# Optimization experiments

Measured on AMD Instinct MI355X. Metric: run time of the kernel, lower is better.

## Reference

```python
import jax, jax.numpy as jnp
import numpy as np

B, S, N = 64, 256, 512


def setup_inputs() -> dict:
    key = jax.random.key(0)
    ks = jax.random.split(key, 8)
    x = jax.random.normal(ks[0], (B, S, N), dtype=jnp.float32)
    # sparse adjacency, no self loops (module assumes adj has no self-loop)
    adj = (jax.random.uniform(ks[1], (N, N)) < 0.05).astype(jnp.float32)
    adj = adj * (1.0 - jnp.eye(N, dtype=jnp.float32))
    W = jax.random.uniform(ks[2], (N, N), dtype=jnp.float32)  # torch.rand init
    parent_node_weigh = jax.random.uniform(ks[3], (N,), dtype=jnp.float32)
    bound = 1.0 / np.sqrt(N)  # torch Linear default init
    Wq_w = jax.random.uniform(ks[4], (N, N), minval=-bound, maxval=bound, dtype=jnp.float32)
    Wq_b = jax.random.uniform(ks[5], (N,), minval=-bound, maxval=bound, dtype=jnp.float32)
    Wk_w = jax.random.uniform(ks[6], (N, N), minval=-bound, maxval=bound, dtype=jnp.float32)
    Wk_b = jax.random.uniform(ks[7], (N,), minval=-bound, maxval=bound, dtype=jnp.float32)
    return {"x": x, "adj": adj, "W": W, "parent_node_weigh": parent_node_weigh,
            "Wq_w": Wq_w, "Wq_b": Wq_b, "Wk_w": Wk_w, "Wk_b": Wk_b}


def reference(x, adj, W, parent_node_weigh, Wq_w, Wq_b, Wk_w, Wk_b):
    # x: (B,S,N). Q,K = Linear(x).permute(0,2,1) -> (B,N,S)
    Q = jnp.einsum('bsk,nk->bns', x, Wq_w) + Wq_b[None, :, None]
    K = jnp.einsum('bsk,nk->bns', x, Wk_w) + Wk_b[None, :, None]
    xt = jnp.transpose(x, (0, 2, 1))  # (B,N,S)
    n = adj.shape[0]
    # Algebraic equivalent of the repeat/mask/matmul/bmm chain:
    # Att[b,m,n] = adj[m,n] * sum_j W[m,j] * adj[j,n] * <K[b,j,:], Q[b,n,:]>
    S_kq = jnp.einsum('bjs,bns->bjn', K, Q)  # (B,N,N)
    Att = adj * jnp.einsum('mj,bjn->bmn', W, adj[:, :, None].transpose(2, 0, 1)[0][None] * S_kq if False else adj[None, :, :] * S_kq)
    Att = Att + jnp.diag(parent_node_weigh)[None, :, :]
    cycle_adj = jnp.eye(n, dtype=adj.dtype) + adj
    Att = jax.nn.softmax(Att, axis=1) * cycle_adj  # softmax over dim=1 (torch dim=1)
    agg_x = jnp.einsum('bmn,bms->bns', Att, xt)  # Att^T @ x
    return (agg_x, Att)
```

## Files before the change

kernel.cpp:

```cpp
#include <hip/hip_runtime.h>
#include <hip/hip_fp16.h>
#include <cstdint>
#include <cmath>

#define BB 64
#define SS 256
#define NN 512
#define MAXC 64

typedef float f32x4 __attribute__((ext_vector_type(4)));
typedef _Float16 half8 __attribute__((ext_vector_type(8)));
typedef _Float16 h2 __attribute__((ext_vector_type(2)));

__device__ __forceinline__ unsigned short f2h(float f) {
  return __half_as_ushort(__float2half(f));
}
__device__ __forceinline__ h2 u2h2(uint32_t u) {
  union { uint32_t u; h2 h; } c; c.u = u; return c.h;
}
__device__ __forceinline__ float2 unpackh2(uint32_t u) {
  return make_float2(__half2float(__ushort_as_half((unsigned short)(u & 0xffffu))),
                     __half2float(__ushort_as_half((unsigned short)(u >> 16))));
}

__device__ __forceinline__ void gload_lds16(const void* g, void* s) {
  __builtin_amdgcn_global_load_lds(
      (const __attribute__((address_space(1))) uint32_t*)g,
      (__attribute__((address_space(3))) uint32_t*)s, 16, 0, 0);
}

__global__ __launch_bounds__(256) void k_collist(const float* __restrict__ adj,
                                                 int* __restrict__ col_idx,
                                                 int* __restrict__ col_cnt) {
  const int n = blockIdx.x * 4 + (threadIdx.x >> 6);
  const int lane = threadIdx.x & 63;
  int cnt = 0;
  for (int m0 = 0; m0 < NN; m0 += 64) {
    const int m = m0 + lane;
    const float a = adj[(size_t)m * NN + n];
    unsigned long long mask = __ballot(a != 0.0f);
    const int prefix = __popcll(mask & ((1ull << lane) - 1ull));
    if (a != 0.0f && cnt + prefix < MAXC) col_idx[n * MAXC + cnt + prefix] = m;
    cnt += __popcll(mask);
  }
  if (lane == 0) col_cnt[n] = (cnt > MAXC) ? MAXC : cnt;
}

__global__ __launch_bounds__(256) void k_wsub(const float* __restrict__ W,
                                              const int* __restrict__ col_idx,
                                              const int* __restrict__ col_cnt,
                                              int* __restrict__ col_off,
                                              float* __restrict__ Wsub) {
  const int n = blockIdx.x;
  const int t = threadIdx.x;
  const int wave = t >> 6, lane = t & 63;
  __shared__ int lsh[MAXC];
  __shared__ int preSh;
  const int c = col_cnt[n];
  if (wave == 0) {
    int pre = 0;
#pragma unroll
    for (int i0 = 0; i0 < NN; i0 += 64) {
      const int i = i0 + lane;
      const int cc = col_cnt[i];
      pre += (i < n) ? cc * cc : 0;
    }
#pragma unroll
    for (int off = 32; off; off >>= 1) pre += __shfl_xor(pre, off);
    if (lane == 0) { col_off[n] = pre; preSh = pre; }
    if (lane < c) lsh[lane] = col_idx[n * MAXC + lane];
  }
  __syncthreads();
  if (lane < c) {
    const float* Wm = W + (size_t)lsh[lane] * NN;
    float* dst = Wsub + preSh + lane;
    for (int ji = wave; ji < c; ji += 4)
      dst[(size_t)ji * c] = Wm[lsh[ji]];
  }
}

__global__ __launch_bounds__(256) void k_xprep(const float* __restrict__ x,
                                               unsigned short* __restrict__ xp,
                                               unsigned short* __restrict__ xt,
                                               float* __restrict__ Att) {
  __shared__ float tile[32][33];
  const int b = blockIdx.z;
  const int s0 = blockIdx.x * 32, n0 = blockIdx.y * 32;
  const float* xb = x + (size_t)b * SS * NN;
  const int tx = threadIdx.x, ty = threadIdx.y;
#pragma unroll
  for (int i = ty; i < 32; i += 8) {
    const float v = xb[(size_t)(s0 + i) * NN + n0 + tx];
    tile[i][tx] = v;
    xp[(size_t)(b * SS + s0 + i) * 512 + n0 + tx] = f2h(v);
  }
  {
    const int bid = (blockIdx.z * 16 + blockIdx.y) * 8 + blockIdx.x;
    const int t = ty * 32 + tx;
    f32x4* dst = (f32x4*)(Att + (size_t)bid * 2048);
    const f32x4 z = (f32x4)0.0f;
    dst[t] = z;
    dst[t + 256] = z;
  }
  __syncthreads();
  unsigned short* xtb = xt + (size_t)b * NN * SS;
#pragma unroll
  for (int i = ty; i < 32; i += 8)
    xtb[(size_t)(n0 + i) * SS + s0 + tx] = f2h(tile[tx][i]);
}

__global__ __launch_bounds__(128) void k_wsplit(const float* __restrict__ Wq,
                                                const float* __restrict__ Wk,
                                                unsigned short* __restrict__ Wqp,
                                                unsigned short* __restrict__ Wkp) {
  const int n = blockIdx.x;
  const float* src = blockIdx.y ? Wk : Wq;
  unsigned short* dst = blockIdx.y ? Wkp : Wqp;
  const int k = threadIdx.x * 4;
  float4 v = *(const float4*)(src + (size_t)n * NN + k);
  ushort4 o;
  o.x = f2h(v.x); o.y = f2h(v.y); o.z = f2h(v.z); o.w = f2h(v.w);
  *(ushort4*)(dst + (size_t)n * 512 + k) = o;
}

__global__ __launch_bounds__(256, 2) void k_lin2(const unsigned short* __restrict__ Wqp,
                                                 const unsigned short* __restrict__ Wkp,
                                                 const float* __restrict__ bq,
                                                 const float* __restrict__ bk,
                                                 const unsigned short* __restrict__ xp,
                                                 unsigned short* __restrict__ Qt,
                                                 unsigned short* __restrict__ Kt) {
  __shared__ __align__(16) char sm[49152];
  const int t = threadIdx.x;
  const int w = t >> 6, l = t & 63;
  const int id = blockIdx.x;
  const int xcd = id & 7, sub = id >> 3;
  const int bn0 = (xcd * 16 + (sub >> 2)) * 128;
  const int bm0 = (sub & 3) * 128;

  const int swz = (((l & 3) ^ ((l >> 3) & 3))) * 16;
  const char* srcb[6];
  char* dstb[6];
#pragma unroll
  for (int i = 0; i < 6; i++) {
    const int ch = w * 6 + i;
    const int panel = ch >> 3, rowgrp = ch & 7;
    const int row = rowgrp * 16 + (l >> 2);
    const char* g0 = (panel == 0) ? (const char*)Wqp
                   : (panel == 1) ? (const char*)Wkp : (const char*)xp;
    const int gr = ((panel == 2) ? bn0 : bm0) + row;
    srcb[i] = g0 + (size_t)gr * 1024 + swz;
    dstb[i] = sm + panel * 8192 + rowgrp * 1024 + l * 16;
  }

  const int fr = l & 15, fg = l >> 4;
  const int mrow = (w >> 1) * 64, ncol = (w & 1) * 64;
  const int slot = (fg ^ ((fr >> 1) & 3)) * 16;
  int offQ[4], offK[4], offB[4];
#pragma unroll
  for (int fm = 0; fm < 4; fm++) {
    offQ[fm] = (mrow + fm * 16 + fr) * 64 + slot;
    offK[fm] = 8192 + (mrow + fm * 16 + fr) * 64 + slot;
    offB[fm] = 16384 + (ncol + fm * 16 + fr) * 64 + slot;
  }

  f32x4 accq[4][4], acck[4][4];
#pragma unroll
  for (int i = 0; i < 4; i++)
#pragma unroll
    for (int j = 0; j < 4; j++) { accq[i][j] = (f32x4)0.0f; acck[i][j] = (f32x4)0.0f; }

#pragma unroll
  for (int i = 0; i < 6; i++) gload_lds16(srcb[i], dstb[i]);
  __syncthreads();

  int cur = 0;
  for (int kk = 0; kk < 16; kk++) {
    if (kk + 1 < 16) {
      const int ko = (kk + 1) * 64;
      const int boff = (cur ^ 1) * 24576;
#pragma unroll
      for (int i = 0; i < 6; i++)
        gload_lds16(srcb[i] + ko, dstb[i] + boff);
    }
    const char* base = sm + cur * 24576;
    half8 afq[4], afk[4];
#pragma unroll
    for (int fm = 0; fm < 4; fm++) {
      afq[fm] = *(const half8*)(base + offQ[fm]);
      afk[fm] = *(const half8*)(base + offK[fm]);
    }
#pragma unroll
    for (int fn = 0; fn < 4; fn++) {
      const half8 bv = *(const half8*)(base + offB[fn]);
#pragma unroll
      for (int fm = 0; fm < 4; fm++) {
        accq[fm][fn] = __builtin_amdgcn_mfma_f32_16x16x32_f16(afq[fm], bv, accq[fm][fn], 0, 0, 0);
        acck[fm][fn] = __builtin_amdgcn_mfma_f32_16x16x32_f16(afk[fm], bv, acck[fm][fn], 0, 0, 0);
      }
    }
    __syncthreads();
    cur ^= 1;
  }

  const int b = bn0 >> 8;
  const int sbase = (bn0 & 255) + ncol;
#pragma unroll
  for (int fm = 0; fm < 4; fm++) {
#pragma unroll
    for (int q = 0; q < 4; q++) {
      const int n = bm0 + mrow + fm * 16 + fg * 4 + q;
      const float bvq = bq[n];
      const float bvk = bk[n];
#pragma unroll
      for (int fn = 0; fn < 4; fn++) {
        const int s = sbase + fn * 16 + fr;
        Qt[((size_t)b * NN + n) * SS + s] = f2h(accq[fm][fn][q] + bvq);
        Kt[((size_t)b * NN + n) * SS + s] = f2h(acck[fm][fn][q] + bvk);
      }
    }
  }
}

__global__ __launch_bounds__(256) void k_fused(const unsigned short* __restrict__ Qt,
                                               const unsigned short* __restrict__ Kt,
                                               const unsigned short* __restrict__ xt,
                                               const float* __restrict__ Wsub,
                                               const float* __restrict__ pnw,
                                               const int* __restrict__ col_idx,
                                               const int* __restrict__ col_cnt,
                                               const int* __restrict__ col_off,
                                               float* __restrict__ Att,
                                               float* __restrict__ agg) {
  const int id = blockIdx.x;
  const int xcd = id & 7;
  const int r = id >> 3;
  const int n = r & 511;
  const int bgrp = r >> 9;
  const int t = threadIdx.x;
  const int wave = t >> 6, lane = t & 63;
  const int b = (xcd << 3) + (bgrp << 2) + wave;

  __shared__ int   lsh[MAXC + 1];
  __shared__ int   lshB[MAXC + 1];
  __shared__ float Wsh[MAXC * MAXC];
  __shared__ float vsh[4][MAXC];
  __shared__ float ash[4][MAXC + 1];

  const int c = col_cnt[n];
  if (t < c) {
    const int v = col_idx[n * MAXC + t];
    lsh[t] = v;
    lshB[t] = v << 9;
  }
  if (t == c) { lsh[c] = n; lshB[c] = n << 9; }
  {
    const int cc = c * c;
    const float* Wp = Wsub + col_off[n];
    for (int i = t; i < cc; i += 256) Wsh[i] = Wp[i];
  }
  __syncthreads();

  const int g = lane >> 4, q = lane & 15;
  const unsigned short* Qrow = Qt + ((size_t)b * NN + n) * SS;
  const char* Kb = (const char*)(Kt + (size_t)b * NN * SS);
  h2 qh[4][2];
#pragma unroll
  for (int u = 0; u < 4; u++) {
    const uint2 v = *(const uint2*)(Qrow + (u * 16 + q) * 4);
    qh[u][0] = u2h2(v.x);
    qh[u][1] = u2h2(v.y);
  }
  for (int j0 = 0; j0 < c; j0 += 4) {
    const int ji = j0 + g;
    float p = 0.0f;
    if (ji < c) {
      const char* Krow = Kb + lshB[ji];
#pragma unroll
      for (int u = 0; u < 4; u++) {
        const uint2 kv = *(const uint2*)(Krow + u * 128 + q * 8);
        p = __builtin_amdgcn_fdot2(u2h2(kv.x), qh[u][0], p, false);
        p = __builtin_amdgcn_fdot2(u2h2(kv.y), qh[u][1], p, false);
      }
    }
    p += __shfl_down(p, 8, 16);
    p += __shfl_down(p, 4, 16);
    p += __shfl_down(p, 2, 16);
    p += __shfl_down(p, 1, 16);
    if (q == 0 && ji < c) vsh[wave][ji] = p;
  }

  float aval = 0.0f;
  if (lane < c) {
    for (int ji = 0; ji < c; ji++)
      aval += Wsh[ji * c + lane] * vsh[wave][ji];
  }

  const float dlg = pnw[n];
  float mval = (lane < c) ? aval : -INFINITY;
#pragma unroll
  for (int off = 32; off; off >>= 1) mval = fmaxf(mval, __shfl_xor(mval, off));
  const float colmax = fmaxf(mval, fmaxf(dlg, 0.0f));
  const float e = (lane < c) ? __expf(aval - colmax) : 0.0f;
  float sum = e;
#pragma unroll
  for (int off = 32; off; off >>= 1) sum += __shfl_xor(sum, off);
  const float denom = sum + __expf(dlg - colmax)
                    + (float)(NN - c - 1) * __expf(-colmax);
  const float inv = 1.0f / denom;

  float* Acol = Att + (size_t)b * NN * NN + n;
  if (lane < c) {
    const float attv = e * inv;
    ash[wave][lane] = attv;
    Acol[(size_t)lsh[lane] * NN] = attv;
  }
  if (lane == c) {
    const float dv = __expf(dlg - colmax) * inv;
    ash[wave][c] = dv;
    Acol[(size_t)n * NN] = dv;
  }

  const char* xtb = (const char*)(xt + (size_t)b * NN * SS);
  f32x4 acc = (f32x4)0.0f;
  for (int mi = 0; mi <= c; mi++) {
    const float a = ash[wave][mi];
    const uint2 v = *(const uint2*)(xtb + lshB[mi] + lane * 8);
    const float2 x01 = unpackh2(v.x);
    const float2 x23 = unpackh2(v.y);
    acc.x += a * x01.x;
    acc.y += a * x01.y;
    acc.z += a * x23.x;
    acc.w += a * x23.y;
  }
  *(f32x4*)(agg + ((size_t)b * NN + n) * SS + lane * 4) = acc;
}

extern "C" void kernel_launch(void* const* d_in, const int* in_sizes, int n_in,
                              void* d_out, int out_size, void* d_ws, size_t ws_size,
                              hipStream_t stream) {
  const float* x    = (const float*)d_in[0];
  const float* adj  = (const float*)d_in[1];
  const float* W    = (const float*)d_in[2];
  const float* pnw  = (const float*)d_in[3];
  const float* Wq_w = (const float*)d_in[4];
  const float* Wq_b = (const float*)d_in[5];
  const float* Wk_w = (const float*)d_in[6];
  const float* Wk_b = (const float*)d_in[7];

  float* agg = (float*)d_out;
  float* Att = (float*)d_out + (size_t)BB * NN * SS;

  char* p = (char*)d_ws;
  unsigned short* xp  = (unsigned short*)p; p += (size_t)BB * SS * 512 * 2;
  unsigned short* Wqp = (unsigned short*)p; p += (size_t)NN * 512 * 2;
  unsigned short* Wkp = (unsigned short*)p; p += (size_t)NN * 512 * 2;
  unsigned short* Qt  = (unsigned short*)p; p += (size_t)BB * NN * SS * 2;
  unsigned short* Kt  = (unsigned short*)p; p += (size_t)BB * NN * SS * 2;
  unsigned short* xt  = (unsigned short*)p; p += (size_t)BB * NN * SS * 2;
  float* Wsub = (float*)p; p += (size_t)NN * MAXC * MAXC * 4;
  int* col_idx = (int*)p; p += (size_t)NN * MAXC * 4;
  int* col_cnt = (int*)p; p += NN * 4;
  int* col_off = (int*)p;

  k_collist<<<dim3(NN / 4), dim3(256), 0, stream>>>(adj, col_idx, col_cnt);
  k_wsub<<<dim3(NN), dim3(256), 0, stream>>>(W, col_idx, col_cnt, col_off, Wsub);
  k_xprep<<<dim3(SS / 32, NN / 32, BB), dim3(32, 8), 0, stream>>>(x, xp, xt, Att);
  k_wsplit<<<dim3(NN, 2), dim3(128), 0, stream>>>(Wq_w, Wk_w, Wqp, Wkp);

  k_lin2<<<dim3(512), dim3(256), 0, stream>>>(Wqp, Wkp, Wq_b, Wk_b, xp, Qt, Kt);
  k_fused<<<dim3(8192), dim3(256), 0, stream>>>(Qt, Kt, xt, Wsub, pnw,
                                                col_idx, col_cnt, col_off,
                                                Att, agg);
}
```

Measured before the change: 123.8 us.

## Precompute dense Q·K Gram matrix with MFMA instead of sparse per-neighbor dot products

```diff
diff --git a/kernel.cpp b/kernel.cpp
--- a/kernel.cpp
+++ b/kernel.cpp
@@ -10,13 +10,12 @@
 
 typedef float f32x4 __attribute__((ext_vector_type(4)));
 typedef _Float16 half8 __attribute__((ext_vector_type(8)));
-typedef _Float16 h2 __attribute__((ext_vector_type(2)));
 
 __device__ __forceinline__ unsigned short f2h(float f) {
   return __half_as_ushort(__float2half(f));
 }
-__device__ __forceinline__ h2 u2h2(uint32_t u) {
-  union { uint32_t u; h2 h; } c; c.u = u; return c.h;
+__device__ __forceinline__ float h2f(unsigned short u) {
+  return __half2float(__ushort_as_half(u));
 }
 __device__ __forceinline__ float2 unpackh2(uint32_t u) {
   return make_float2(__half2float(__ushort_as_half((unsigned short)(u & 0xffffu))),
@@ -222,8 +221,94 @@
   }
 }
 
-__global__ __launch_bounds__(256) void k_fused(const unsigned short* __restrict__ Qt,
-                                               const unsigned short* __restrict__ Kt,
+__global__ __launch_bounds__(256, 2) void k_gram(const unsigned short* __restrict__ Qt,
+                                                 const unsigned short* __restrict__ Kt,
+                                                 unsigned short* __restrict__ ST) {
+  __shared__ __align__(16) char sm[32768];
+  const int t = threadIdx.x;
+  const int w = t >> 6, l = t & 63;
+  const int id = blockIdx.x;
+  const int xcd = id & 7, rest = id >> 3;
+  const int batch = (xcd << 3) + (rest >> 4);
+  const int tile = rest & 15;
+  const int m0 = (tile >> 2) * 128;
+  const int n0 = (tile & 3) * 128;
+
+  const int swz = (((l & 3) ^ ((l >> 3) & 3))) * 16;
+  const char* srcb[4];
+  char* dstb[4];
+#pragma unroll
+  for (int i = 0; i < 4; i++) {
+    const int ch = w * 4 + i;
+    const int panel = ch >> 3, rowgrp = ch & 7;
+    const int row = rowgrp * 16 + (l >> 2);
+    const char* g0 = panel ? (const char*)Kt : (const char*)Qt;
+    const int gr = (panel ? n0 : m0) + row;
+    srcb[i] = g0 + ((size_t)batch * 512 + gr) * 512 + swz;
+    dstb[i] = sm + panel * 8192 + rowgrp * 1024 + l * 16;
+  }
+
+  const int fr = l & 15, fg = l >> 4;
+  const int mrow = (w >> 1) * 64, ncol = (w & 1) * 64;
+  const int slot = (fg ^ ((fr >> 1) & 3)) * 16;
+  int offA[4], offB[4];
+#pragma unroll
+  for (int fm = 0; fm < 4; fm++) {
+    offA[fm] = (mrow + fm * 16 + fr) * 64 + slot;
+    offB[fm] = 8192 + (ncol + fm * 16 + fr) * 64 + slot;
+  }
+
+  f32x4 acc[4][4];
+#pragma unroll
+  for (int i = 0; i < 4; i++)
+#pragma unroll
+    for (int j = 0; j < 4; j++) acc[i][j] = (f32x4)0.0f;
+
+#pragma unroll
+  for (int i = 0; i < 4; i++) gload_lds16(srcb[i], dstb[i]);
+  __syncthreads();
+
+  int cur = 0;
+  for (int kk = 0; kk < 8; kk++) {
+    if (kk + 1 < 8) {
+      const int ko = (kk + 1) * 64;
+      const int boff = (cur ^ 1) * 16384;
+#pragma unroll
+      for (int i = 0; i < 4; i++)
+        gload_lds16(srcb[i] + ko, dstb[i] + boff);
+    }
+    const char* base = sm + cur * 16384;
+    half8 af[4];
+#pragma unroll
+    for (int fm = 0; fm < 4; fm++)
+      af[fm] = *(const half8*)(base + offA[fm]);
+#pragma unroll
+    for (int fn = 0; fn < 4; fn++) {
+      const half8 bv = *(const half8*)(base + offB[fn]);
+#pragma unroll
+      for (int fm = 0; fm < 4; fm++)
+        acc[fm][fn] = __builtin_amdgcn_mfma_f32_16x16x32_f16(af[fm], bv, acc[fm][fn], 0, 0, 0);
+    }
+    __syncthreads();
+    cur ^= 1;
+  }
+
+  unsigned short* STb = ST + (size_t)batch * NN * NN;
+#pragma unroll
+  for (int fm = 0; fm < 4; fm++) {
+#pragma unroll
+    for (int q = 0; q < 4; q++) {
+      const int n = m0 + mrow + fm * 16 + fg * 4 + q;
+#pragma unroll
+      for (int fn = 0; fn < 4; fn++) {
+        const int j = n0 + ncol + fn * 16 + fr;
+        STb[(size_t)n * NN + j] = f2h(acc[fm][fn][q]);
+      }
+    }
+  }
+}
+
+__global__ __launch_bounds__(256) void k_fused(const unsigned short* __restrict__ ST,
                                                const unsigned short* __restrict__ xt,
                                                const float* __restrict__ Wsub,
                                                const float* __restrict__ pnw,
@@ -261,34 +346,8 @@
   }
   __syncthreads();
 
-  const int g = lane >> 4, q = lane & 15;
-  const unsigned short* Qrow = Qt + ((size_t)b * NN + n) * SS;
-  const char* Kb = (const char*)(Kt + (size_t)b * NN * SS);
-  h2 qh[4][2];
-#pragma unroll
-  for (int u = 0; u < 4; u++) {
-    const uint2 v = *(const uint2*)(Qrow + (u * 16 + q) * 4);
-    qh[u][0] = u2h2(v.x);
-    qh[u][1] = u2h2(v.y);
-  }
-  for (int j0 = 0; j0 < c; j0 += 4) {
-    const int ji = j0 + g;
-    float p = 0.0f;
-    if (ji < c) {
-      const char* Krow = Kb + lshB[ji];
-#pragma unroll
-      for (int u = 0; u < 4; u++) {
-        const uint2 kv = *(const uint2*)(Krow + u * 128 + q * 8);
-        p = __builtin_amdgcn_fdot2(u2h2(kv.x), qh[u][0], p, false);
-        p = __builtin_amdgcn_fdot2(u2h2(kv.y), qh[u][1], p, false);
-      }
-    }
-    p += __shfl_down(p, 8, 16);
-    p += __shfl_down(p, 4, 16);
-    p += __shfl_down(p, 2, 16);
-    p += __shfl_down(p, 1, 16);
-    if (q == 0 && ji < c) vsh[wave][ji] = p;
-  }
+  const unsigned short* STrow = ST + ((size_t)b * NN + n) * NN;
+  if (lane < c) vsh[wave][lane] = h2f(STrow[lsh[lane]]);
 
   float aval = 0.0f;
   if (lane < c) {
@@ -358,6 +417,7 @@
   unsigned short* Qt  = (unsigned short*)p; p += (size_t)BB * NN * SS * 2;
   unsigned short* Kt  = (unsigned short*)p; p += (size_t)BB * NN * SS * 2;
   unsigned short* xt  = (unsigned short*)p; p += (size_t)BB * NN * SS * 2;
+  unsigned short* ST  = (unsigned short*)p; p += (size_t)BB * NN * NN * 2;
   float* Wsub = (float*)p; p += (size_t)NN * MAXC * MAXC * 4;
   int* col_idx = (int*)p; p += (size_t)NN * MAXC * 4;
   int* col_cnt = (int*)p; p += NN * 4;
@@ -369,7 +429,8 @@
   k_wsplit<<<dim3(NN, 2), dim3(128), 0, stream>>>(Wq_w, Wk_w, Wqp, Wkp);
 
   k_lin2<<<dim3(512), dim3(256), 0, stream>>>(Wqp, Wkp, Wq_b, Wk_b, xp, Qt, Kt);
-  k_fused<<<dim3(8192), dim3(256), 0, stream>>>(Qt, Kt, xt, Wsub, pnw,
+  k_gram<<<dim3(1024), dim3(256), 0, stream>>>(Qt, Kt, ST);
+  k_fused<<<dim3(8192), dim3(256), 0, stream>>>(ST, xt, Wsub, pnw,
                                                 col_idx, col_cnt, col_off,
                                                 Att, agg);
 }
```

Result: faster. 117.0 us (-5.5%).
